# Performance work log

Hardware: AMD Instinct MI355X
Metric: run time of the kernel (lower is better)

Reference implementation:

```python
import jax, jax.numpy as jnp
import numpy as np

B, N, D = 4, 2048, 512
H = 8
HD = D // H
MLP_H = 4 * D
SCALE = HD ** -0.5
ELEV_SCALE = 1000.0
EPS = 1e-5


def _ln(x, g, b):
    m = jnp.mean(x, axis=-1, keepdims=True)
    v = jnp.mean((x - m) ** 2, axis=-1, keepdims=True)
    return (x - m) * jax.lax.rsqrt(v + EPS) * g + b


def setup_inputs() -> dict:
    key = jax.random.key(0)
    ks = jax.random.split(key, 10)
    s = lambda fin: (2.0 / fin) ** 0.5
    return {
        "x": jax.random.normal(ks[0], (B, N, D), jnp.float32),
        "elevation_patches": jax.random.uniform(ks[1], (B, N), jnp.float32) * 3000.0,
        "ln1_g": jnp.ones((D,), jnp.float32),
        "ln1_b": jnp.zeros((D,), jnp.float32),
        "qkv_w": jax.random.normal(ks[2], (D, 3 * D), jnp.float32) * s(D),
        "alpha": jnp.ones((1,), jnp.float32),
        "proj_w": jax.random.normal(ks[3], (D, D), jnp.float32) * s(D),
        "proj_b": jnp.zeros((D,), jnp.float32),
        "ln2_g": jnp.ones((D,), jnp.float32),
        "ln2_b": jnp.zeros((D,), jnp.float32),
        "fc1_w": jax.random.normal(ks[4], (D, MLP_H), jnp.float32) * s(D),
        "fc1_b": jnp.zeros((MLP_H,), jnp.float32),
        "fc2_w": jax.random.normal(ks[5], (MLP_H, D), jnp.float32) * s(MLP_H),
        "fc2_b": jnp.zeros((D,), jnp.float32),
    }


def reference(x, elevation_patches, ln1_g, ln1_b, qkv_w, alpha, proj_w, proj_b,
              ln2_g, ln2_b, fc1_w, fc1_b, fc2_w, fc2_b):
    # --- attention ---
    h = _ln(x, ln1_g, ln1_b)
    qkv = (h @ qkv_w).reshape(B, N, 3, H, HD)
    q, k, v = (jnp.moveaxis(qkv[:, :, i], 1, 2) for i in range(3))  # [B,H,N,HD]
    scores = jnp.einsum('bhnd,bhmd->bhnm', q, k) * SCALE
    elev_diff = (elevation_patches[:, None, :] - elevation_patches[:, :, None]) / ELEV_SCALE
    bias = jnp.clip(-alpha[0] * jax.nn.relu(elev_diff), -10.0, 0.0)  # [B,N,N]
    attn = jax.nn.softmax(scores + bias[:, None], axis=-1)
    out = jnp.einsum('bhnm,bhmd->bhnd', attn, v)
    out = jnp.moveaxis(out, 1, 2).reshape(B, N, D) @ proj_w + proj_b
    x = x + out
    # --- mlp ---
    h2 = _ln(x, ln2_g, ln2_b)
    mlp = jax.nn.gelu(h2 @ fc1_w + fc1_b, approximate=False) @ fc2_w + fc2_b
    return x + mlp
```

## Files before the change

kernel.cpp:

```cpp
#include <hip/hip_runtime.h>
#include <math.h>

typedef unsigned short u16;
typedef unsigned int u32;

#define B_ 4
#define N_ 2048
#define D_ 512
#define H_ 8
#define HD_ 64
#define MLP_H_ 2048
#define EPS_ 1e-5f
#define C2_ 14.426950408889634f
#define QSCALE_ 0.1803368801111204f
#define EL2_ 0.0014426950408889634f

#if __has_builtin(__builtin_amdgcn_exp2f)
#define EXP2(x) __builtin_amdgcn_exp2f(x)
#else
#define EXP2(x) exp2f(x)
#endif

__device__ __forceinline__ u16 bf16_rne(float x) {
  u32 u = __float_as_uint(x);
  u32 r = (u + 0x7FFFu + ((u >> 16) & 1u)) >> 16;
  return (u16)r;
}
#if __has_builtin(__builtin_amdgcn_cvt_pk_bf16_f32)
typedef __bf16 bf2_t __attribute__((ext_vector_type(2)));
__device__ __forceinline__ u32 pk_bf16(float a, float b) {
  bf2_t v = __builtin_amdgcn_cvt_pk_bf16_f32(a, b);
  u32 r; __builtin_memcpy(&r, &v, 4); return r;
}
#else
__device__ __forceinline__ u32 pk_bf16(float a, float b) {
  return (u32)bf16_rne(a) | ((u32)bf16_rne(b) << 16);
}
#endif
__device__ __forceinline__ void bf16_split(float x, u16& h, u16& l) {
  h = bf16_rne(x);
  float hf = __uint_as_float(((u32)h) << 16);
  l = bf16_rne(x - hf);
}

typedef __attribute__((ext_vector_type(8))) short bfrag;
typedef __attribute__((ext_vector_type(4))) float ffrag;

#define LDS_AS(p) ((__attribute__((address_space(3))) void*)(p))
#define GLB_AS(p) ((const __attribute__((address_space(1))) void*)(p))

__global__ __launch_bounds__(256) void ln_kernel(
    const float* __restrict__ x, const float* __restrict__ g,
    const float* __restrict__ b, u16* __restrict__ o)
{
  __shared__ float red[8];
  int row = blockIdx.x;
  int tid = threadIdx.x;
  const float* xr = x + (size_t)row * D_;
  float v0 = xr[tid], v1 = xr[tid + 256];
  float s = v0 + v1;
  #pragma unroll
  for (int off = 32; off > 0; off >>= 1) s += __shfl_xor(s, off, 64);
  if ((tid & 63) == 0) red[tid >> 6] = s;
  __syncthreads();
  float mean = (red[0] + red[1] + red[2] + red[3]) * (1.0f / D_);
  float d0 = v0 - mean, d1 = v1 - mean;
  float vs = d0 * d0 + d1 * d1;
  #pragma unroll
  for (int off = 32; off > 0; off >>= 1) vs += __shfl_xor(vs, off, 64);
  if ((tid & 63) == 0) red[4 + (tid >> 6)] = vs;
  __syncthreads();
  float var = (red[4] + red[5] + red[6] + red[7]) * (1.0f / D_);
  float r = rsqrtf(var + EPS_);
  u16* orow = o + (size_t)row * D_;
  orow[tid]       = bf16_rne(d0 * r * g[tid] + b[tid]);
  orow[tid + 256] = bf16_rne(d1 * r * g[tid + 256] + b[tid + 256]);
}

__global__ __launch_bounds__(256) void e2_kernel(
    const float* __restrict__ elev, const float* __restrict__ alpha,
    float* __restrict__ e2)
{
  int i = blockIdx.x * 256 + threadIdx.x;
  e2[i] = elev[i] * (alpha[0] * EL2_);
}

__global__ __launch_bounds__(256) void wsplit_kernel(
    const float* __restrict__ W, u16* __restrict__ Thi, u16* __restrict__ Tlo,
    int K, int N)
{
  __shared__ float tile[64][65];
  int n0 = blockIdx.x * 64, k0 = blockIdx.y * 64;
  int c = threadIdx.x & 63, r4 = threadIdx.x >> 6;
  #pragma unroll
  for (int i = 0; i < 16; i++) {
    int r = r4 + i * 4;
    tile[r][c] = W[(size_t)(k0 + r) * N + n0 + c];
  }
  __syncthreads();
  #pragma unroll
  for (int i = 0; i < 16; i++) {
    int rn = r4 + i * 4;
    float v = tile[c][rn];
    size_t o = (size_t)(n0 + rn) * K + k0 + c;
    if (Tlo) {
      u16 h, l; bf16_split(v, h, l);
      Thi[o] = h; Tlo[o] = l;
    } else {
      Thi[o] = bf16_rne(v);
    }
  }
}

template<int ROWS>
__device__ __forceinline__ void stage32(const u16* __restrict__ src, int ld,
                                        int r0, int k0, u16* lds, int lane, int wave)
{
  #pragma unroll
  for (int i = 0; i < ROWS / 64; i++) {
    int seg = wave * (ROWS / 64) + i;
    int chunk = seg * 64 + lane;
    int r = chunk >> 2;
    int c = (chunk & 3) ^ ((r >> 1) & 3);
    const u16* g = src + (size_t)(r0 + r) * ld + k0 + c * 8;
    __builtin_amdgcn_global_load_lds(GLB_AS(g), LDS_AS((char*)lds + seg * 1024), 16, 0, 0);
  }
}

__device__ __forceinline__ int swz_off(int R, int quad) {
  return R * 32 + ((quad ^ ((R >> 1) & 3)) * 8);
}

template<int TBM, int TBN, int WR, int WC, int TERMS>
__global__ __launch_bounds__(256) void gemm_tpl(
    const u16* __restrict__ Ahi,
    const u16* __restrict__ Whi, const u16* __restrict__ Wlo,
    const float* __restrict__ bias, const float* __restrict__ res,
    float* __restrict__ Cf, u16* __restrict__ Ohi, u16* __restrict__ Olo,
    int M, int K, int N, int act, int qcols)
{
  constexpr int MF = TBM / (WR * 16);
  constexpr int NF = TBN / (WC * 16);
  __shared__ __align__(16) u16 As[2][TBM * 32];
  __shared__ __align__(16) u16 Bh[2][TBN * 32];
  __shared__ __align__(16) u16 Bl[(TERMS >= 2) ? 2 : 1][(TERMS >= 2) ? TBN * 32 : 8];

  int tid = threadIdx.x;
  int lane = tid & 63, wave = tid >> 6;
  int wr = wave / WC, wc = wave % WC;
  int ln = lane & 15, quad = lane >> 4;
  int m0 = blockIdx.y * TBM, n0 = blockIdx.x * TBN;

  ffrag acc[MF][NF] = {};

  for (int k0 = 0; k0 < K; k0 += 64) {
    stage32<TBM>(Ahi, K, m0, k0,      As[0], lane, wave);
    stage32<TBM>(Ahi, K, m0, k0 + 32, As[1], lane, wave);
    stage32<TBN>(Whi, K, n0, k0,      Bh[0], lane, wave);
    stage32<TBN>(Whi, K, n0, k0 + 32, Bh[1], lane, wave);
    if constexpr (TERMS >= 2) {
      stage32<TBN>(Wlo, K, n0, k0,      Bl[0], lane, wave);
      stage32<TBN>(Wlo, K, n0, k0 + 32, Bl[1], lane, wave);
    }
    __syncthreads();

    #pragma unroll
    for (int hf = 0; hf < 2; hf++) {
      bfrag ah[MF], bh[NF], bl[NF];
      #pragma unroll
      for (int t = 0; t < MF; t++)
        ah[t] = *(const bfrag*)(As[hf] + swz_off(wr * (TBM / WR) + t * 16 + ln, quad));
      #pragma unroll
      for (int u = 0; u < NF; u++) {
        int off = swz_off(wc * (TBN / WC) + u * 16 + ln, quad);
        bh[u] = *(const bfrag*)(Bh[hf] + off);
        if constexpr (TERMS >= 2) bl[u] = *(const bfrag*)(Bl[hf] + off);
      }
      #pragma unroll
      for (int ti = 0; ti < MF; ti++) {
        #pragma unroll
        for (int tj = 0; tj < NF; tj++) {
          acc[ti][tj] = __builtin_amdgcn_mfma_f32_16x16x32_bf16(ah[ti], bh[tj], acc[ti][tj], 0, 0, 0);
          if constexpr (TERMS >= 2)
            acc[ti][tj] = __builtin_amdgcn_mfma_f32_16x16x32_bf16(ah[ti], bl[tj], acc[ti][tj], 0, 0, 0);
        }
      }
    }
    __syncthreads();
  }

  #pragma unroll
  for (int tj = 0; tj < NF; tj++) {
    int col = n0 + wc * (TBN / WC) + tj * 16 + ln;
    float bv = bias ? bias[col] : 0.f;
    float cs = (col < qcols) ? QSCALE_ : 1.0f;
    bool store_lo = (col < qcols);
    #pragma unroll
    for (int ti = 0; ti < MF; ti++) {
      int rw = m0 + wr * (TBM / WR) + ti * 16 + quad * 4;
      #pragma unroll
      for (int r = 0; r < 4; r++) {
        float y = acc[ti][tj][r] + bv;
        if (act) y = 0.5f * y * (1.f + erff(y * 0.70710678118654752f));
        if (res) y += res[(size_t)(rw + r) * N + col];
        if (Cf) Cf[(size_t)(rw + r) * N + col] = y;
        if (Ohi) {
          y *= cs;
          if (Olo && store_lo) {
            u16 hh, ll; bf16_split(y, hh, ll);
            Ohi[(size_t)(rw + r) * N + col] = hh;
            Olo[(size_t)(rw + r) * N + col] = ll;
          } else {
            Ohi[(size_t)(rw + r) * N + col] = bf16_rne(y);
          }
        }
      }
    }
  }
}

__global__ __launch_bounds__(256) void vtrans_kernel(
    const u16* __restrict__ qh, u16* __restrict__ vth)
{
  __shared__ u16 Th[64][72];
  int b = blockIdx.z, h = blockIdx.y, n0 = blockIdx.x * 64;
  int t = threadIdx.x;
  int nr = t >> 2, ds = (t & 3) * 16;
  size_t src = ((size_t)(b * N_ + n0 + nr)) * 1536 + 1024 + h * 64 + ds;
  *(uint4*)&Th[nr][ds]     = *(const uint4*)(qh + src);
  *(uint4*)&Th[nr][ds + 8] = *(const uint4*)(qh + src + 8);
  __syncthreads();
  int dr = t >> 2, ns = (t & 3) * 16;
  u16 oh[16];
  #pragma unroll
  for (int j = 0; j < 16; j++) oh[j] = Th[ns + j][dr];
  size_t dst = ((size_t)((b * H_ + h) * 64 + dr)) * N_ + n0 + ns;
  *(uint4*)(vth + dst)     = *(uint4*)(oh);
  *(uint4*)(vth + dst + 8) = *(uint4*)(oh + 8);
}

__device__ __forceinline__ void stage_tile64(const u16* __restrict__ gbase, size_t rstride,
                                             u16* lds, int wave, int lane)
{
  #pragma unroll
  for (int i = 0; i < 2; i++) {
    int seg = wave * 2 + i;
    int chunk = seg * 64 + lane;
    int ch = chunk >> 8;
    int pc = chunk & 255;
    int r = pc >> 2;
    int q = (pc & 3) ^ ((r >> 1) & 3);
    const u16* g = gbase + (size_t)r * rstride + ch * 32 + q * 8;
    __builtin_amdgcn_global_load_lds(GLB_AS(g), LDS_AS((char*)lds + seg * 1024), 16, 0, 0);
  }
}

__device__ __forceinline__ int frag_off(int c, int R, int quad) {
  return c * 2048 + R * 32 + ((quad ^ ((R >> 1) & 3)) * 8);
}

__global__ __launch_bounds__(256) void attn_mfma_kernel(
    const u16* __restrict__ qkh, const u16* __restrict__ qkl,
    const u16* __restrict__ vth,
    const float* __restrict__ e2, u16* __restrict__ outb)
{
  __shared__ __align__(16) u16 Kh[4096];
  __shared__ __align__(16) u16 Vh[4096];
  __shared__ __align__(16) u16 Pw[4][16][72];

  int b = blockIdx.z, h = blockIdx.y;
  int q0 = blockIdx.x * 64;
  int tid = threadIdx.x;
  int lane = tid & 63, wq = tid >> 6;
  int ln = lane & 15, quad = lane >> 4;

  const u16* qb_h = qkh + ((size_t)(b * N_ + q0)) * 1536 + h * 64;
  const u16* qb_l = qkl + ((size_t)(b * N_ + q0)) * 1536 + h * 64;
  stage_tile64(qb_h, 1536, Kh, wq, lane);
  stage_tile64(qb_l, 1536, Vh, wq, lane);
  __syncthreads();

  bfrag qfh[2], qfl[2];
  #pragma unroll
  for (int c = 0; c < 2; c++) {
    int off = frag_off(c, wq * 16 + ln, quad);
    qfh[c] = *(const bfrag*)(Kh + off);
    qfl[c] = *(const bfrag*)(Vh + off);
  }
  __syncthreads();

  float e2q = e2[b * N_ + q0 + wq * 16 + ln];
  float m_i = -3.0e38f, l_i = 0.f;
  ffrag O[4] = {};

  const u16* kp = qkh + (size_t)b * N_ * 1536 + 512 + h * 64;
  const u16* vp = vth + (size_t)(b * H_ + h) * 64 * N_;
  const float* ep = e2 + b * N_;

  for (int k0 = 0; k0 < N_; k0 += 64) {
    stage_tile64(kp, 1536, Kh, wq, lane);
    stage_tile64(vp, N_, Vh, wq, lane);
    kp += (size_t)64 * 1536;
    vp += 64;
    __syncthreads();

    ffrag S[4];
    #pragma unroll
    for (int kt = 0; kt < 4; kt++) {
      ffrag s = {0.f, 0.f, 0.f, 0.f};
      #pragma unroll
      for (int c = 0; c < 2; c++) {
        bfrag kf = *(const bfrag*)(Kh + frag_off(c, kt * 16 + ln, quad));
        s = __builtin_amdgcn_mfma_f32_16x16x32_bf16(kf, qfh[c], s, 0, 0, 0);
        s = __builtin_amdgcn_mfma_f32_16x16x32_bf16(kf, qfl[c], s, 0, 0, 0);
      }
      S[kt] = s;
    }

    float4 ek[4];
    #pragma unroll
    for (int kt = 0; kt < 4; kt++)
      ek[kt] = *(const float4*)&ep[k0 + kt * 16 + quad * 4];

    float p[4][4];
    float mx = -3.0e38f;
    #pragma unroll
    for (int kt = 0; kt < 4; kt++) {
      #pragma unroll
      for (int r = 0; r < 4; r++) {
        float d = (&ek[kt].x)[r] - e2q;
        d = fminf(fmaxf(d, 0.f), C2_);
        float sv = S[kt][r] - d;
        p[kt][r] = sv;
        mx = fmaxf(mx, sv);
      }
    }
    mx = fmaxf(mx, __shfl_xor(mx, 16, 64));
    mx = fmaxf(mx, __shfl_xor(mx, 32, 64));
    float mnew = fmaxf(m_i, mx);
    float corr = EXP2(m_i - mnew);
    float ps = 0.f;
    #pragma unroll
    for (int kt = 0; kt < 4; kt++) {
      #pragma unroll
      for (int r = 0; r < 4; r++) {
        float pv = EXP2(p[kt][r] - mnew);
        p[kt][r] = pv;
        ps += pv;
      }
    }
    ps += __shfl_xor(ps, 16, 64);
    ps += __shfl_xor(ps, 32, 64);
    m_i = mnew;
    l_i = l_i * corr + ps;
    #pragma unroll
    for (int dt = 0; dt < 4; dt++) O[dt] *= corr;

    #pragma unroll
    for (int kt = 0; kt < 4; kt++) {
      u32 w0 = pk_bf16(p[kt][0], p[kt][1]);
      u32 w1 = pk_bf16(p[kt][2], p[kt][3]);
      *(uint2*)&Pw[wq][ln][kt * 16 + quad * 4] = make_uint2(w0, w1);
    }

    bfrag pf[2];
    #pragma unroll
    for (int c = 0; c < 2; c++)
      pf[c] = *(const bfrag*)&Pw[wq][ln][c * 32 + quad * 8];

    #pragma unroll
    for (int dt = 0; dt < 4; dt++) {
      ffrag o = O[dt];
      #pragma unroll
      for (int c = 0; c < 2; c++) {
        bfrag vf = *(const bfrag*)(Vh + frag_off(c, dt * 16 + ln, quad));
        o = __builtin_amdgcn_mfma_f32_16x16x32_bf16(vf, pf[c], o, 0, 0, 0);
      }
      O[dt] = o;
    }
    __syncthreads();
  }

  float inv = 1.0f / l_i;
  int row = q0 + wq * 16 + ln;
  #pragma unroll
  for (int dt = 0; dt < 4; dt++) {
    u32 w0 = pk_bf16(O[dt][0] * inv, O[dt][1] * inv);
    u32 w1 = pk_bf16(O[dt][2] * inv, O[dt][3] * inv);
    *(uint2*)&outb[((size_t)(b * N_ + row)) * D_ + h * 64 + dt * 16 + quad * 4] =
        make_uint2(w0, w1);
  }
}

extern "C" void kernel_launch(void* const* d_in, const int* in_sizes, int n_in,
                              void* d_out, int out_size, void* d_ws, size_t ws_size,
                              hipStream_t stream) {
  const float* x      = (const float*)d_in[0];
  const float* elev   = (const float*)d_in[1];
  const float* ln1_g  = (const float*)d_in[2];
  const float* ln1_b  = (const float*)d_in[3];
  const float* qkv_w  = (const float*)d_in[4];
  const float* alpha  = (const float*)d_in[5];
  const float* proj_w = (const float*)d_in[6];
  const float* proj_b = (const float*)d_in[7];
  const float* ln2_g  = (const float*)d_in[8];
  const float* ln2_b  = (const float*)d_in[9];
  const float* fc1_w  = (const float*)d_in[10];
  const float* fc1_b  = (const float*)d_in[11];
  const float* fc2_w  = (const float*)d_in[12];
  const float* fc2_b  = (const float*)d_in[13];
  float* out = (float*)d_out;

  const size_t HBf   = (size_t)B_ * N_ * D_;
  const size_t QKVE  = (size_t)B_ * N_ * 3 * D_;
  const size_t MLPE  = (size_t)B_ * N_ * MLP_H_;

  char* p = (char*)d_ws;
  u16* abuf = (u16*)p;                     p += HBf * 2;
  char* region = p;                        p += QKVE * 4;
  u16* qkvh   = (u16*)region;
  u16* qkvl   = (u16*)(region + QKVE * 2);
  u16* mlp_hi = (u16*)region;
  u16* vth  = (u16*)p;  p += HBf * 2;
  float* xres = (float*)p;                 p += HBf * 4;
  u16* qw_hi = (u16*)p;  p += (size_t)D_ * 3 * D_ * 2;
  u16* qw_lo = (u16*)p;  p += (size_t)D_ * 3 * D_ * 2;
  u16* pw_hi = (u16*)p;  p += (size_t)D_ * D_ * 2;
  u16* f1_hi = (u16*)p;  p += (size_t)D_ * MLP_H_ * 2;
  u16* f2_hi = (u16*)p;  p += (size_t)MLP_H_ * D_ * 2;
  float* e2  = (float*)p; p += (size_t)B_ * N_ * 4;

  const int rows = B_ * N_;

  wsplit_kernel<<<dim3(3 * D_ / 64, D_ / 64), 256, 0, stream>>>(qkv_w, qw_hi, qw_lo, D_, 3 * D_);
  wsplit_kernel<<<dim3(D_ / 64, D_ / 64), 256, 0, stream>>>(proj_w, pw_hi, nullptr, D_, D_);
  wsplit_kernel<<<dim3(MLP_H_ / 64, D_ / 64), 256, 0, stream>>>(fc1_w, f1_hi, nullptr, D_, MLP_H_);
  wsplit_kernel<<<dim3(D_ / 64, MLP_H_ / 64), 256, 0, stream>>>(fc2_w, f2_hi, nullptr, MLP_H_, D_);
  e2_kernel<<<rows / 256, 256, 0, stream>>>(elev, alpha, e2);

  ln_kernel<<<rows, 256, 0, stream>>>(x, ln1_g, ln1_b, abuf);
  gemm_tpl<128, 128, 2, 2, 2><<<dim3(1536 / 128, rows / 128), 256, 0, stream>>>(
      abuf, qw_hi, qw_lo, nullptr, nullptr,
      nullptr, qkvh, qkvl, rows, D_, 1536, 0, D_);
  vtrans_kernel<<<dim3(N_ / 64, H_, B_), 256, 0, stream>>>(qkvh, vth);
  attn_mfma_kernel<<<dim3(N_ / 64, H_, B_), 256, 0, stream>>>(
      qkvh, qkvl, vth, e2, abuf);
  gemm_tpl<64, 128, 1, 4, 1><<<dim3(D_ / 128, rows / 64), 256, 0, stream>>>(
      abuf, pw_hi, nullptr, proj_b, x,
      xres, nullptr, nullptr, rows, D_, D_, 0, 0);
  ln_kernel<<<rows, 256, 0, stream>>>(xres, ln2_g, ln2_b, abuf);
  gemm_tpl<128, 128, 2, 2, 1><<<dim3(MLP_H_ / 128, rows / 128), 256, 0, stream>>>(
      abuf, f1_hi, nullptr, fc1_b, nullptr,
      nullptr, mlp_hi, nullptr, rows, D_, MLP_H_, 1, 0);
  gemm_tpl<64, 128, 1, 4, 1><<<dim3(D_ / 128, rows / 64), 256, 0, stream>>>(
      mlp_hi, f2_hi, nullptr, fc2_b, xres,
      out, nullptr, nullptr, rows, MLP_H_, D_, 0, 0);
}
```

Baseline: 427.0 us.

## Write V transposed from a separate GEMM and merge weight prep launches

The QKV projection is split in two. A 2-term GEMM now produces only Q and K, and a 1-term GEMM with a new epilogue writes V directly in the transposed [B,H,HD,N] layout the attention kernel reads. This removes the separate vtrans kernel, the hi/lo split work and storage for V, and the 1536-wide intermediate rows. The four weight-conversion launches become one, and the elevation pre-scale is folded into the first layernorm, cutting launch count. The V epilogue writes scattered 8-byte stores, which may coalesce poorly. The extra GEMM launch re-reads the normalized activations.

```diff
diff --git a/kernel.cpp b/kernel.cpp
--- a/kernel.cpp
+++ b/kernel.cpp
@@ -51,11 +51,14 @@
 
 __global__ __launch_bounds__(256) void ln_kernel(
     const float* __restrict__ x, const float* __restrict__ g,
-    const float* __restrict__ b, u16* __restrict__ o)
+    const float* __restrict__ b, u16* __restrict__ o,
+    const float* __restrict__ elev, const float* __restrict__ alpha,
+    float* __restrict__ e2)
 {
   __shared__ float red[8];
   int row = blockIdx.x;
   int tid = threadIdx.x;
+  if (e2 && tid == 0) e2[row] = elev[row] * (alpha[0] * EL2_);
   const float* xr = x + (size_t)row * D_;
   float v0 = xr[tid], v1 = xr[tid + 256];
   float s = v0 + v1;
@@ -77,21 +80,13 @@
   orow[tid + 256] = bf16_rne(d1 * r * g[tid + 256] + b[tid + 256]);
 }
 
-__global__ __launch_bounds__(256) void e2_kernel(
-    const float* __restrict__ elev, const float* __restrict__ alpha,
-    float* __restrict__ e2)
-{
-  int i = blockIdx.x * 256 + threadIdx.x;
-  e2[i] = elev[i] * (alpha[0] * EL2_);
-}
-
-__global__ __launch_bounds__(256) void wsplit_kernel(
+__device__ __forceinline__ void wsplit_body(
     const float* __restrict__ W, u16* __restrict__ Thi, u16* __restrict__ Tlo,
-    int K, int N)
+    int K, int N, int bx, int by, int tid)
 {
   __shared__ float tile[64][65];
-  int n0 = blockIdx.x * 64, k0 = blockIdx.y * 64;
-  int c = threadIdx.x & 63, r4 = threadIdx.x >> 6;
+  int n0 = bx * 64, k0 = by * 64;
+  int c = tid & 63, r4 = tid >> 6;
   #pragma unroll
   for (int i = 0; i < 16; i++) {
     int r = r4 + i * 4;
@@ -112,6 +107,28 @@
   }
 }
 
+__global__ __launch_bounds__(256) void wsplit_all(
+    const float* __restrict__ qkv_w, const float* __restrict__ proj_w,
+    const float* __restrict__ fc1_w, const float* __restrict__ fc2_w,
+    u16* __restrict__ qw_hi, u16* __restrict__ qw_lo,
+    u16* __restrict__ pw_hi, u16* __restrict__ f1_hi, u16* __restrict__ f2_hi)
+{
+  int id = blockIdx.x;
+  int tid = threadIdx.x;
+  if (id < 192) {
+    wsplit_body(qkv_w, qw_hi, qw_lo, 512, 1536, id % 24, id / 24, tid);
+  } else if (id < 256) {
+    int l = id - 192;
+    wsplit_body(proj_w, pw_hi, nullptr, 512, 512, l % 8, l / 8, tid);
+  } else if (id < 512) {
+    int l = id - 256;
+    wsplit_body(fc1_w, f1_hi, nullptr, 512, 2048, l % 32, l / 32, tid);
+  } else {
+    int l = id - 512;
+    wsplit_body(fc2_w, f2_hi, nullptr, 2048, 512, l % 8, l / 8, tid);
+  }
+}
+
 template<int ROWS>
 __device__ __forceinline__ void stage32(const u16* __restrict__ src, int ld,
                                         int r0, int k0, u16* lds, int lane, int wave)
@@ -131,7 +148,7 @@
   return R * 32 + ((quad ^ ((R >> 1) & 3)) * 8);
 }
 
-template<int TBM, int TBN, int WR, int WC, int TERMS>
+template<int TBM, int TBN, int WR, int WC, int TERMS, int VT>
 __global__ __launch_bounds__(256) void gemm_tpl(
     const u16* __restrict__ Ahi,
     const u16* __restrict__ Whi, const u16* __restrict__ Wlo,
@@ -141,9 +158,14 @@
 {
   constexpr int MF = TBM / (WR * 16);
   constexpr int NF = TBN / (WC * 16);
-  __shared__ __align__(16) u16 As[2][TBM * 32];
-  __shared__ __align__(16) u16 Bh[2][TBN * 32];
-  __shared__ __align__(16) u16 Bl[(TERMS >= 2) ? 2 : 1][(TERMS >= 2) ? TBN * 32 : 8];
+  constexpr int AT = TBM * 32;
+  constexpr int BT = TBN * 32;
+  constexpr int SMEMU = 2 * AT + ((TERMS >= 2) ? 4 * BT : 2 * BT);
+  __shared__ __align__(16) u16 smem[SMEMU];
+  u16* As0 = smem;               u16* As1 = smem + AT;
+  u16* Bh0 = smem + 2 * AT;      u16* Bh1 = smem + 2 * AT + BT;
+  u16* Bl0 = smem + 2 * AT + 2 * BT;
+  u16* Bl1 = smem + 2 * AT + 3 * BT;
 
   int tid = threadIdx.x;
   int lane = tid & 63, wave = tid >> 6;
@@ -154,27 +176,30 @@
   ffrag acc[MF][NF] = {};
 
   for (int k0 = 0; k0 < K; k0 += 64) {
-    stage32<TBM>(Ahi, K, m0, k0,      As[0], lane, wave);
-    stage32<TBM>(Ahi, K, m0, k0 + 32, As[1], lane, wave);
-    stage32<TBN>(Whi, K, n0, k0,      Bh[0], lane, wave);
-    stage32<TBN>(Whi, K, n0, k0 + 32, Bh[1], lane, wave);
+    stage32<TBM>(Ahi, K, m0, k0,      As0, lane, wave);
+    stage32<TBM>(Ahi, K, m0, k0 + 32, As1, lane, wave);
+    stage32<TBN>(Whi, K, n0, k0,      Bh0, lane, wave);
+    stage32<TBN>(Whi, K, n0, k0 + 32, Bh1, lane, wave);
     if constexpr (TERMS >= 2) {
-      stage32<TBN>(Wlo, K, n0, k0,      Bl[0], lane, wave);
-      stage32<TBN>(Wlo, K, n0, k0 + 32, Bl[1], lane, wave);
+      stage32<TBN>(Wlo, K, n0, k0,      Bl0, lane, wave);
+      stage32<TBN>(Wlo, K, n0, k0 + 32, Bl1, lane, wave);
     }
     __syncthreads();
 
     #pragma unroll
     for (int hf = 0; hf < 2; hf++) {
+      const u16* Asf = hf ? As1 : As0;
+      const u16* Bhf = hf ? Bh1 : Bh0;
+      const u16* Blf = hf ? Bl1 : Bl0;
       bfrag ah[MF], bh[NF], bl[NF];
       #pragma unroll
       for (int t = 0; t < MF; t++)
-        ah[t] = *(const bfrag*)(As[hf] + swz_off(wr * (TBM / WR) + t * 16 + ln, quad));
+        ah[t] = *(const bfrag*)(Asf + swz_off(wr * (TBM / WR) + t * 16 + ln, quad));
       #pragma unroll
       for (int u = 0; u < NF; u++) {
         int off = swz_off(wc * (TBN / WC) + u * 16 + ln, quad);
-        bh[u] = *(const bfrag*)(Bh[hf] + off);
-        if constexpr (TERMS >= 2) bl[u] = *(const bfrag*)(Bl[hf] + off);
+        bh[u] = *(const bfrag*)(Bhf + off);
+        if constexpr (TERMS >= 2) bl[u] = *(const bfrag*)(Blf + off);
       }
       #pragma unroll
       for (int ti = 0; ti < MF; ti++) {
@@ -187,6 +212,24 @@
       }
     }
     __syncthreads();
+  }
+
+  if constexpr (VT) {
+    #pragma unroll
+    for (int tj = 0; tj < NF; tj++) {
+      int col = n0 + wc * (TBN / WC) + tj * 16 + ln;
+      int h = col >> 6, d = col & 63;
+      #pragma unroll
+      for (int ti = 0; ti < MF; ti++) {
+        int rw = m0 + wr * (TBM / WR) + ti * 16 + quad * 4;
+        int bb = rw >> 11, n = rw & (N_ - 1);
+        u32 w0 = pk_bf16(acc[ti][tj][0], acc[ti][tj][1]);
+        u32 w1 = pk_bf16(acc[ti][tj][2], acc[ti][tj][3]);
+        size_t dst = ((size_t)((bb * H_ + h) * HD_ + d)) * N_ + n;
+        *(uint2*)(Ohi + dst) = make_uint2(w0, w1);
+      }
+    }
+    return;
   }
 
   #pragma unroll
@@ -219,26 +262,6 @@
   }
 }
 
-__global__ __launch_bounds__(256) void vtrans_kernel(
-    const u16* __restrict__ qh, u16* __restrict__ vth)
-{
-  __shared__ u16 Th[64][72];
-  int b = blockIdx.z, h = blockIdx.y, n0 = blockIdx.x * 64;
-  int t = threadIdx.x;
-  int nr = t >> 2, ds = (t & 3) * 16;
-  size_t src = ((size_t)(b * N_ + n0 + nr)) * 1536 + 1024 + h * 64 + ds;
-  *(uint4*)&Th[nr][ds]     = *(const uint4*)(qh + src);
-  *(uint4*)&Th[nr][ds + 8] = *(const uint4*)(qh + src + 8);
-  __syncthreads();
-  int dr = t >> 2, ns = (t & 3) * 16;
-  u16 oh[16];
-  #pragma unroll
-  for (int j = 0; j < 16; j++) oh[j] = Th[ns + j][dr];
-  size_t dst = ((size_t)((b * H_ + h) * 64 + dr)) * N_ + n0 + ns;
-  *(uint4*)(vth + dst)     = *(uint4*)(oh);
-  *(uint4*)(vth + dst + 8) = *(uint4*)(oh + 8);
-}
-
 __device__ __forceinline__ void stage_tile64(const u16* __restrict__ gbase, size_t rstride,
                                              u16* lds, int wave, int lane)
 {
@@ -274,10 +297,10 @@
   int lane = tid & 63, wq = tid >> 6;
   int ln = lane & 15, quad = lane >> 4;
 
-  const u16* qb_h = qkh + ((size_t)(b * N_ + q0)) * 1536 + h * 64;
-  const u16* qb_l = qkl + ((size_t)(b * N_ + q0)) * 1536 + h * 64;
-  stage_tile64(qb_h, 1536, Kh, wq, lane);
-  stage_tile64(qb_l, 1536, Vh, wq, lane);
+  const u16* qb_h = qkh + ((size_t)(b * N_ + q0)) * 1024 + h * 64;
+  const u16* qb_l = qkl + ((size_t)(b * N_ + q0)) * 1024 + h * 64;
+  stage_tile64(qb_h, 1024, Kh, wq, lane);
+  stage_tile64(qb_l, 1024, Vh, wq, lane);
   __syncthreads();
 
   bfrag qfh[2], qfl[2];
@@ -293,14 +316,14 @@
   float m_i = -3.0e38f, l_i = 0.f;
   ffrag O[4] = {};
 
-  const u16* kp = qkh + (size_t)b * N_ * 1536 + 512 + h * 64;
-  const u16* vp = vth + (size_t)(b * H_ + h) * 64 * N_;
+  const u16* kp = qkh + (size_t)b * N_ * 1024 + 512 + h * 64;
+  const u16* vp = vth + (size_t)(b * H_ + h) * HD_ * N_;
   const float* ep = e2 + b * N_;
 
   for (int k0 = 0; k0 < N_; k0 += 64) {
-    stage_tile64(kp, 1536, Kh, wq, lane);
+    stage_tile64(kp, 1024, Kh, wq, lane);
     stage_tile64(vp, N_, Vh, wq, lane);
-    kp += (size_t)64 * 1536;
+    kp += (size_t)64 * 1024;
     vp += 64;
     __syncthreads();
 
@@ -411,15 +434,15 @@
   const float* fc2_b  = (const float*)d_in[13];
   float* out = (float*)d_out;
 
-  const size_t HBf   = (size_t)B_ * N_ * D_;
-  const size_t QKVE  = (size_t)B_ * N_ * 3 * D_;
-  const size_t MLPE  = (size_t)B_ * N_ * MLP_H_;
+  const size_t HBf  = (size_t)B_ * N_ * D_;
+  const size_t QKE  = (size_t)B_ * N_ * 1024;
+  const size_t MLPE = (size_t)B_ * N_ * MLP_H_;
 
   char* p = (char*)d_ws;
   u16* abuf = (u16*)p;                     p += HBf * 2;
-  char* region = p;                        p += QKVE * 4;
-  u16* qkvh   = (u16*)region;
-  u16* qkvl   = (u16*)(region + QKVE * 2);
+  char* region = p;                        p += MLPE * 2;
+  u16* qkh    = (u16*)region;
+  u16* qkl    = (u16*)(region + QKE * 2);
   u16* mlp_hi = (u16*)region;
   u16* vth  = (u16*)p;  p += HBf * 2;
   float* xres = (float*)p;                 p += HBf * 4;
@@ -432,27 +455,25 @@
 
   const int rows = B_ * N_;
 
-  wsplit_kernel<<<dim3(3 * D_ / 64, D_ / 64), 256, 0, stream>>>(qkv_w, qw_hi, qw_lo, D_, 3 * D_);
-  wsplit_kernel<<<dim3(D_ / 64, D_ / 64), 256, 0, stream>>>(proj_w, pw_hi, nullptr, D_, D_);
-  wsplit_kernel<<<dim3(MLP_H_ / 64, D_ / 64), 256, 0, stream>>>(fc1_w, f1_hi, nullptr, D_, MLP_H_);
-  wsplit_kernel<<<dim3(D_ / 64, MLP_H_ / 64), 256, 0, stream>>>(fc2_w, f2_hi, nullptr, MLP_H_, D_);
-  e2_kernel<<<rows / 256, 256, 0, stream>>>(elev, alpha, e2);
-
-  ln_kernel<<<rows, 256, 0, stream>>>(x, ln1_g, ln1_b, abuf);
-  gemm_tpl<128, 128, 2, 2, 2><<<dim3(1536 / 128, rows / 128), 256, 0, stream>>>(
+  wsplit_all<<<768, 256, 0, stream>>>(qkv_w, proj_w, fc1_w, fc2_w,
+                                      qw_hi, qw_lo, pw_hi, f1_hi, f2_hi);
+  ln_kernel<<<rows, 256, 0, stream>>>(x, ln1_g, ln1_b, abuf, elev, alpha, e2);
+  gemm_tpl<128, 128, 2, 2, 2, 0><<<dim3(1024 / 128, rows / 128), 256, 0, stream>>>(
       abuf, qw_hi, qw_lo, nullptr, nullptr,
-      nullptr, qkvh, qkvl, rows, D_, 1536, 0, D_);
-  vtrans_kernel<<<dim3(N_ / 64, H_, B_), 256, 0, stream>>>(qkvh, vth);
+      nullptr, qkh, qkl, rows, D_, 1024, 0, D_);
+  gemm_tpl<64, 128, 1, 4, 1, 1><<<dim3(512 / 128, rows / 64), 256, 0, stream>>>(
+      abuf, qw_hi + (size_t)1024 * D_, nullptr, nullptr, nullptr,
+      nullptr, vth, nullptr, rows, D_, 512, 0, 0);
   attn_mfma_kernel<<<dim3(N_ / 64, H_, B_), 256, 0, stream>>>(
-      qkvh, qkvl, vth, e2, abuf);
-  gemm_tpl<64, 128, 1, 4, 1><<<dim3(D_ / 128, rows / 64), 256, 0, stream>>>(
+      qkh, qkl, vth, e2, abuf);
+  gemm_tpl<64, 128, 1, 4, 1, 0><<<dim3(D_ / 128, rows / 64), 256, 0, stream>>>(
       abuf, pw_hi, nullptr, proj_b, x,
       xres, nullptr, nullptr, rows, D_, D_, 0, 0);
-  ln_kernel<<<rows, 256, 0, stream>>>(xres, ln2_g, ln2_b, abuf);
-  gemm_tpl<128, 128, 2, 2, 1><<<dim3(MLP_H_ / 128, rows / 128), 256, 0, stream>>>(
+  ln_kernel<<<rows, 256, 0, stream>>>(xres, ln2_g, ln2_b, abuf, nullptr, nullptr, nullptr);
+  gemm_tpl<128, 128, 2, 2, 1, 0><<<dim3(MLP_H_ / 128, rows / 128), 256, 0, stream>>>(
       abuf, f1_hi, nullptr, fc1_b, nullptr,
       nullptr, mlp_hi, nullptr, rows, D_, MLP_H_, 1, 0);
-  gemm_tpl<64, 128, 1, 4, 1><<<dim3(D_ / 128, rows / 64), 256, 0, stream>>>(
+  gemm_tpl<64, 128, 1, 4, 1, 0><<<dim3(D_ / 128, rows / 64), 256, 0, stream>>>(
       mlp_hi, f2_hi, nullptr, fc2_b, xres,
       out, nullptr, nullptr, rows, MLP_H_, D_, 0, 0);
 }
```

Result: faster. 404.2 us (-5.3%).
